# Kernel optimization log

Hardware: AMD Instinct MI355X
Metric: run time of the kernel (lower is better)

Reference implementation:

```python
import jax, jax.numpy as jnp
import numpy as np

TOKEN_SIZE = 4
NEIGHBOR_SIZE = 3


def setup_inputs() -> dict:
    key = jax.random.key(0)
    ks = jax.random.split(key, 8)
    B, C, H, W = 8, 256, 64, 64
    return {
        "blue_feat": jax.random.normal(ks[0], (B, C, H, W), jnp.float32),
        "white_feat": jax.random.normal(ks[1], (B, C, H, W), jnp.float32),
        "Wq": jax.random.normal(ks[2], (C, C), jnp.float32) * 0.05,
        "bq": jax.random.normal(ks[3], (C,), jnp.float32) * 0.05,
        "Wk": jax.random.normal(ks[4], (C, C), jnp.float32) * 0.05,
        "bk": jax.random.normal(ks[5], (C,), jnp.float32) * 0.05,
        "Wv": jax.random.normal(ks[6], (C, C), jnp.float32) * 0.05,
        "bv": jax.random.normal(ks[7], (C,), jnp.float32) * 0.05,
    }


def _tokens(x, nh, nw, ts):
    # [B,C,H,W] -> [B,nh,nw,C,ts*ts]
    B, C = x.shape[0], x.shape[1]
    return (x.reshape(B, C, nh, ts, nw, ts)
             .transpose(0, 2, 4, 1, 3, 5)
             .reshape(B, nh, nw, C, ts * ts))


def reference(blue_feat, white_feat, Wq, bq, Wk, bk, Wv, bv):
    ts, ns = TOKEN_SIZE, NEIGHBOR_SIZE
    pad = ns // 2
    B, C, H, W = blue_feat.shape
    scale = float((ts * ts) ** -0.5)

    # 1x1 conv projections (pointwise channel mix + bias)
    Q = jnp.einsum('bchw,oc->bohw', blue_feat, Wq) + bq[None, :, None, None]
    K = jnp.einsum('bchw,oc->bohw', white_feat, Wk) + bk[None, :, None, None]
    V = jnp.einsum('bchw,oc->bohw', white_feat, Wv) + bv[None, :, None, None]

    nh, nw = H // ts, W // ts  # H,W divisible by ts -> no padding branch
    Qt = _tokens(Q, nh, nw, ts)  # [B,nh,nw,C,D]
    Kt = _tokens(K, nh, nw, ts)
    Vt = _tokens(V, nh, nw, ts)

    # zero-padded token grid, gather 3x3 neighbor tokens (F.unfold equivalent)
    padw = ((0, 0), (pad, pad), (pad, pad), (0, 0), (0, 0))
    Kp = jnp.pad(Kt, padw)
    Vp = jnp.pad(Vt, padw)
    Knb = jnp.stack([Kp[:, di:di + nh, dj:dj + nw]
                     for di in range(ns) for dj in range(ns)], axis=3)  # [B,nh,nw,9,C,D]
    Vnb = jnp.stack([Vp[:, di:di + nh, dj:dj + nw]
                     for di in range(ns) for dj in range(ns)], axis=3)

    # per-channel attention over neighbor tokens
    attn = jax.nn.softmax(
        jnp.einsum('bhwcd,bhwncd->bhwcn', Qt, Knb) * scale, axis=-1)
    out = jnp.einsum('bhwcn,bhwncd->bhwcd', attn, Vnb)  # [B,nh,nw,C,D]

    enhanced = (out.reshape(B, nh, nw, C, ts, ts)
                   .transpose(0, 3, 1, 4, 2, 5)
                   .reshape(B, C, H, W))
    return blue_feat + enhanced  # out_proj is Identity since c1 == c2
```

## Files before the change

### kernel.cpp

```cpp
#include <hip/hip_runtime.h>
#include <hip/hip_bf16.h>
#include <stdint.h>

typedef float  f32x4  __attribute__((ext_vector_type(4)));
typedef float  f32x2  __attribute__((ext_vector_type(2)));
typedef __bf16 bf16x8 __attribute__((ext_vector_type(8)));

#define LROW 40

__global__ __launch_bounds__(1024) void prep_kernel(
    const float* __restrict__ blue, const float* __restrict__ white,
    const float* __restrict__ Wq, const float* __restrict__ Wk,
    const float* __restrict__ Wv,
    __bf16* __restrict__ Xtb, __bf16* __restrict__ Xtw,
    __bf16* __restrict__ Wbf)
{
  const int bid = blockIdx.x;
  const int tid = threadIdx.x;

  if (bid >= 256) {
    const int t = bid - 256;
    const float* src = (t == 0) ? Wq : (t == 1) ? Wk : Wv;
    __bf16* dst = Wbf + t * 65536;
#pragma unroll
    for (int it = 0; it < 8; ++it) {
      const int idx = it * 8192 + tid * 8;
      f32x4 v0 = *(const f32x4*)(src + idx);
      f32x4 v1 = *(const f32x4*)(src + idx + 4);
      bf16x8 r;
#pragma unroll
      for (int q = 0; q < 4; ++q) { r[q] = (__bf16)v0[q]; r[q + 4] = (__bf16)v1[q]; }
      *(bf16x8*)(dst + idx) = r;
    }
    return;
  }

  const int srcw = bid >> 7;
  const int rem  = bid & 127;
  const int b    = rem >> 4;
  const int ti   = rem & 15;
  const float* X = srcw ? white : blue;
  __bf16*     Xt = srcw ? Xtw : Xtb;

  const int s  = tid & 7;
  const int co = (tid >> 3) & 31;
  const int u  = tid >> 8;

  const float* Xb = X + (size_t)b * (256 * 4096);
  __bf16* Xtb2 = Xt + (size_t)b * 4096 * 256;

#pragma unroll
  for (int it = 0; it < 4; ++it) {
    const int p   = u * 32 + it * 8 + s;
    const int px  = 2 * p;
    const int r   = px >> 6;
    const int col = px & 63;
    const int hw  = (ti * 4 + r) * 64 + col;
    const int d   = r * 4 + (col & 3);
    const int n   = ti * 256 + (col >> 2) * 16 + d;

    bf16x8 e0, e1;
#pragma unroll
    for (int j = 0; j < 8; ++j) {
      const int c = co * 8 + j;
      f32x2 v = *(const f32x2*)(Xb + (size_t)c * 4096 + hw);
      e0[j] = (__bf16)v[0];
      e1[j] = (__bf16)v[1];
    }
    *(bf16x8*)(Xtb2 + (size_t)n * 256 + co * 8)       = e0;
    *(bf16x8*)(Xtb2 + (size_t)(n + 1) * 256 + co * 8) = e1;
  }
}


#define GLOAD16(GS, LD) \
  __builtin_amdgcn_global_load_lds( \
      (const __attribute__((address_space(1))) uint32_t*)(GS), \
      (__attribute__((address_space(3))) uint32_t*)(LD), 16, 0, 0)

__global__ __launch_bounds__(256) void gemm_lds_kernel(
    const __bf16* __restrict__ Xtb, const __bf16* __restrict__ Xtw,
    const __bf16* __restrict__ Wbf,
    const float* __restrict__ bq, const float* __restrict__ bk,
    const float* __restrict__ bv,
    __bf16* __restrict__ Qt, __bf16* __restrict__ Kt, __bf16* __restrict__ Vt)
{
  __shared__ __bf16 As[3][128 * 32];
  __shared__ __bf16 Bs[3][128 * 32];

  const int bid = blockIdx.x;
  const int lid = (bid & 7) * 192 + (bid >> 3);
  const int nb  = lid / 6;
  const int bt  = lid % 6;
  const int tensor = (bt < 4) ? 1 + (bt & 1) : 0;
  const int ob     = (bt < 4) ? (bt >> 1) : (bt & 1);

  const __bf16* Xt   = (tensor == 0) ? Xtb : Xtw;
  const float*  bias = (tensor == 0) ? bq : (tensor == 1) ? bk : bv;
  __bf16*       Out  = (tensor == 0) ? Qt : (tensor == 1) ? Kt : Vt;
  const __bf16* Wp   = Wbf + tensor * 65536 + ob * 32768;

  const int tid  = threadIdx.x;
  const int lane = tid & 63;
  const int w    = tid >> 6;
  const int wo   = w >> 1;
  const int wn   = w & 1;
  const int lrow = lane & 15;
  const int lks  = lane >> 4;

  const int o0 = ob * 128;
  const int n0 = nb * 128;

  const int l     = lane;
  const int rA    = w * 16 + (l >> 2);
  const int gslot = (l & 3) ^ ((l >> 3) & 3);
  const __bf16* gA = Wp + (size_t)rA * 256 + gslot * 8;
  const __bf16* gB = Xt + (size_t)(n0 + rA) * 256 + gslot * 8;
  const int ldsOffQ0 = (w * 16) * 32;
  const int ldsOffQ1 = (64 + w * 16) * 32;

#define STAGE(BUF, KK) do {                                        \
    GLOAD16(gA + (KK) * 32,             &As[BUF][ldsOffQ0]);       \
    GLOAD16(gA + 64 * 256 + (KK) * 32,  &As[BUF][ldsOffQ1]);       \
    GLOAD16(gB + (KK) * 32,             &Bs[BUF][ldsOffQ0]);       \
    GLOAD16(gB + 64 * 256 + (KK) * 32,  &Bs[BUF][ldsOffQ1]);       \
  } while (0)

  const int sx = ((lks ^ ((lrow >> 1) & 3)) * 8);

  f32x4 acc[4][4];
#pragma unroll
  for (int i = 0; i < 4; ++i)
#pragma unroll
    for (int j = 0; j < 4; ++j) acc[i][j] = (f32x4)0.0f;

#define COMPUTE(BUF) do {                                                       \
    bf16x8 af[4], bfr[4];                                                       \
    _Pragma("unroll")                                                           \
    for (int i = 0; i < 4; ++i)                                                 \
      af[i] = *(const bf16x8*)&As[BUF][(wo * 64 + i * 16 + lrow) * 32 + sx];    \
    _Pragma("unroll")                                                           \
    for (int j = 0; j < 4; ++j)                                                 \
      bfr[j] = *(const bf16x8*)&Bs[BUF][(wn * 64 + j * 16 + lrow) * 32 + sx];   \
    __builtin_amdgcn_s_setprio(1);                                              \
    _Pragma("unroll")                                                           \
    for (int i = 0; i < 4; ++i)                                                 \
      _Pragma("unroll")                                                         \
      for (int j = 0; j < 4; ++j)                                               \
        acc[i][j] = __builtin_amdgcn_mfma_f32_16x16x32_bf16(af[i], bfr[j],      \
                                                            acc[i][j], 0, 0, 0);\
    __builtin_amdgcn_s_setprio(0);                                              \
  } while (0)

  STAGE(0, 0);
  STAGE(1, 1);
  STAGE(2, 2);

#define PHASE(T) do {                                                           \
    if ((T) >= 6) {                                                             \
      if ((T) == 6) asm volatile("s_waitcnt vmcnt(4)" ::: "memory");            \
      else          asm volatile("s_waitcnt vmcnt(0)" ::: "memory");            \
    } else          asm volatile("s_waitcnt vmcnt(8)" ::: "memory");            \
    __builtin_amdgcn_sched_barrier(0);                                          \
    __builtin_amdgcn_s_barrier();                                               \
    __builtin_amdgcn_sched_barrier(0);                                          \
    COMPUTE((T) % 3);                                                           \
    asm volatile("s_waitcnt lgkmcnt(0)" ::: "memory");                          \
    __builtin_amdgcn_sched_barrier(0);                                          \
    __builtin_amdgcn_s_barrier();                                               \
    __builtin_amdgcn_sched_barrier(0);                                          \
    if ((T) < 5) STAGE((T) % 3, (T) + 3);                                       \
  } while (0)

  PHASE(0); PHASE(1); PHASE(2); PHASE(3);
  PHASE(4); PHASE(5); PHASE(6); PHASE(7);
#undef PHASE
#undef STAGE
#undef COMPUTE

#pragma unroll
  for (int i = 0; i < 4; ++i) {
    const int obase = o0 + wo * 64 + i * 16 + (lane >> 4) * 4;
#pragma unroll
    for (int j = 0; j < 4; ++j) {
      const int n  = n0 + wn * 64 + j * 16 + (lane & 15);
      const int bb = n >> 12;
      const int pp = n & 4095;
      const int tt = pp >> 4;
      const int tii = tt >> 4;
      const int tjj = tt & 15;
      const int dd  = pp & 15;
      const size_t base = ((size_t)(bb * 16 + tii) * 256) * 256 + tjj * 16 + dd;
#pragma unroll
      for (int r = 0; r < 4; ++r) {
        const int o = obase + r;
        const float v = acc[i][j][r] + bias[o];
        Out[base + (size_t)o * 256] = (__bf16)v;
      }
    }
  }
}

__global__ __launch_bounds__(256) void proj_gemm_kernel(
    const float* __restrict__ blue, const float* __restrict__ white,
    const float* __restrict__ Wq, const float* __restrict__ bq,
    const float* __restrict__ Wk, const float* __restrict__ bk,
    const float* __restrict__ Wv, const float* __restrict__ bv,
    __bf16* __restrict__ Qt, __bf16* __restrict__ Kt, __bf16* __restrict__ Vt)
{
  __shared__ __bf16 As[128 * LROW];
  __shared__ __bf16 Bs[128 * LROW];

  const int bidhw = blockIdx.x;
  const int lid   = (bidhw & 7) * 192 + (bidhw >> 3);
  const int nb    = lid / 6;
  const int bt    = lid % 6;
  const int tensor = (bt < 4) ? 1 + (bt & 1) : 0;
  const int ob     = (bt < 4) ? (bt >> 1) : (bt & 1);

  const float* X    = (tensor == 0) ? blue : white;
  const float* W    = (tensor == 0) ? Wq : (tensor == 1) ? Wk : Wv;
  const float* bias = (tensor == 0) ? bq : (tensor == 1) ? bk : bv;
  __bf16*      Out  = (tensor == 0) ? Qt : (tensor == 1) ? Kt : Vt;

  const int tid  = threadIdx.x;
  const int lane = tid & 63;
  const int wave = tid >> 6;
  const int wo   = wave >> 1;
  const int wn   = wave & 1;

  const int o0 = ob * 128;
  const int n0 = nb * 128;
  const int batch = n0 >> 12;
  const int p0    = n0 & 4095;
  const int tk0   = p0 >> 4;
  const int trow  = tk0 >> 4;
  const int tcol0 = tk0 & 15;
  const float* Xb = X + (size_t)batch * (256 * 4096);

  f32x4 acc[4][4];
#pragma unroll
  for (int i = 0; i < 4; ++i)
#pragma unroll
    for (int j = 0; j < 4; ++j) acc[i][j] = (f32x4)0.0f;

  const int arow  = tid >> 1;
  const int ahalf = tid & 1;
  const int n2   = tid & 63;
  const int ko   = tid >> 6;
  const int nloc = 2 * n2;
  const int tl   = nloc >> 4;
  const int d    = nloc & 15;
  const int hw   = (trow * 4 + (d >> 2)) * 64 + (tcol0 + tl) * 4 + (d & 3);

  const int lrow = lane & 15;
  const int lk   = (lane >> 4) * 8;

  for (int kk = 0; kk < 8; ++kk) {
    const int k0 = kk * 32;
    {
      const float* src = W + (size_t)(o0 + arow) * 256 + k0 + ahalf * 16;
      f32x4 t0 = *(const f32x4*)(src + 0);
      f32x4 t1 = *(const f32x4*)(src + 4);
      f32x4 t2 = *(const f32x4*)(src + 8);
      f32x4 t3 = *(const f32x4*)(src + 12);
      bf16x8 c0, c1;
#pragma unroll
      for (int qq = 0; qq < 4; ++qq) { c0[qq] = (__bf16)t0[qq]; c0[qq + 4] = (__bf16)t1[qq]; }
#pragma unroll
      for (int qq = 0; qq < 4; ++qq) { c1[qq] = (__bf16)t2[qq]; c1[qq + 4] = (__bf16)t3[qq]; }
      __bf16* dst = As + arow * LROW + ahalf * 16;
      *(bf16x8*)(dst + 0) = c0;
      *(bf16x8*)(dst + 8) = c1;
    }
    {
      const float* src = Xb + (size_t)(k0 + ko * 8) * 4096 + hw;
      f32x2 v0 = *(const f32x2*)(src + 0 * 4096);
      f32x2 v1 = *(const f32x2*)(src + 1 * 4096);
      f32x2 v2 = *(const f32x2*)(src + 2 * 4096);
      f32x2 v3 = *(const f32x2*)(src + 3 * 4096);
      f32x2 v4 = *(const f32x2*)(src + 4 * 4096);
      f32x2 v5 = *(const f32x2*)(src + 5 * 4096);
      f32x2 v6 = *(const f32x2*)(src + 6 * 4096);
      f32x2 v7 = *(const f32x2*)(src + 7 * 4096);
      bf16x8 r0, r1;
      r0[0] = (__bf16)v0[0]; r0[1] = (__bf16)v1[0]; r0[2] = (__bf16)v2[0]; r0[3] = (__bf16)v3[0];
      r0[4] = (__bf16)v4[0]; r0[5] = (__bf16)v5[0]; r0[6] = (__bf16)v6[0]; r0[7] = (__bf16)v7[0];
      r1[0] = (__bf16)v0[1]; r1[1] = (__bf16)v1[1]; r1[2] = (__bf16)v2[1]; r1[3] = (__bf16)v3[1];
      r1[4] = (__bf16)v4[1]; r1[5] = (__bf16)v5[1]; r1[6] = (__bf16)v6[1]; r1[7] = (__bf16)v7[1];
      *(bf16x8*)(Bs + (nloc + 0) * LROW + ko * 8) = r0;
      *(bf16x8*)(Bs + (nloc + 1) * LROW + ko * 8) = r1;
    }
    __syncthreads();

    bf16x8 a[4], b[4];
#pragma unroll
    for (int i = 0; i < 4; ++i)
      a[i] = *(const bf16x8*)(As + (wo * 64 + i * 16 + lrow) * LROW + lk);
#pragma unroll
    for (int j = 0; j < 4; ++j)
      b[j] = *(const bf16x8*)(Bs + (wn * 64 + j * 16 + lrow) * LROW + lk);
#pragma unroll
    for (int i = 0; i < 4; ++i)
#pragma unroll
      for (int j = 0; j < 4; ++j)
        acc[i][j] = __builtin_amdgcn_mfma_f32_16x16x32_bf16(a[i], b[j], acc[i][j], 0, 0, 0);
    __syncthreads();
  }

#pragma unroll
  for (int i = 0; i < 4; ++i) {
    const int obase = o0 + wo * 64 + i * 16 + (lane >> 4) * 4;
#pragma unroll
    for (int j = 0; j < 4; ++j) {
      const int n  = n0 + wn * 64 + j * 16 + (lane & 15);
      const int bb = n >> 12;
      const int p  = n & 4095;
      const int tt = p >> 4;
      const int tii = tt >> 4;
      const int tjj = tt & 15;
      const int dd  = p & 15;
      const size_t base = ((size_t)(bb * 16 + tii) * 256) * 256 + tjj * 16 + dd;
#pragma unroll
      for (int r = 0; r < 4; ++r) {
        const int o = obase + r;
        const float v = acc[i][j][r] + bias[o];
        Out[base + (size_t)o * 256] = (__bf16)v;
      }
    }
  }
}

__device__ __forceinline__ void unpack8(const uint4 v, float* f) {
  const uint32_t u0 = v.x, u1 = v.y, u2 = v.z, u3 = v.w;
  f[0] = __uint_as_float(u0 << 16); f[1] = __uint_as_float(u0 & 0xffff0000u);
  f[2] = __uint_as_float(u1 << 16); f[3] = __uint_as_float(u1 & 0xffff0000u);
  f[4] = __uint_as_float(u2 << 16); f[5] = __uint_as_float(u2 & 0xffff0000u);
  f[6] = __uint_as_float(u3 << 16); f[7] = __uint_as_float(u3 & 0xffff0000u);
}

__global__ __launch_bounds__(256) void attn_kernel(
    const __bf16* __restrict__ Qt, const __bf16* __restrict__ Kt,
    const __bf16* __restrict__ Vt, const float* __restrict__ blue,
    float* __restrict__ out)
{
  const int j   = blockIdx.x;
  const int bid = (j & 7) * 256 + (j >> 3);
  const int cg  = bid & 15;
  const int ti  = (bid >> 4) & 15;
  const int b   = bid >> 8;

  const int tid = threadIdx.x;
  const int tj  = tid & 15;
  const int cl  = tid >> 4;
  const int c   = cg * 16 + cl;

  float q[16];
  {
    const __bf16* p = Qt + ((((size_t)b * 16 + ti) * 256 + c) * 16 + tj) * 16;
    unpack8(*(const uint4*)p, q);
    unpack8(*(const uint4*)(p + 8), q + 8);
  }

  float s[9];
#pragma unroll
  for (int n = 0; n < 9; ++n) {
    const int yi = ti + n / 3 - 1;
    const int yj = tj + n % 3 - 1;
    float dot = 0.0f;
    if (yi >= 0 && yi < 16 && yj >= 0 && yj < 16) {
      const __bf16* p = Kt + ((((size_t)b * 16 + yi) * 256 + c) * 16 + yj) * 16;
      float kf[16];
      unpack8(*(const uint4*)p, kf);
      unpack8(*(const uint4*)(p + 8), kf + 8);
#pragma unroll
      for (int dd = 0; dd < 16; ++dd) dot = fmaf(q[dd], kf[dd], dot);
    }
    s[n] = dot * 0.25f;
  }

  float m = s[0];
#pragma unroll
  for (int n = 1; n < 9; ++n) m = fmaxf(m, s[n]);
  float w[9], denom = 0.0f;
#pragma unroll
  for (int n = 0; n < 9; ++n) { w[n] = __expf(s[n] - m); denom += w[n]; }
  const float inv = 1.0f / denom;

  float o16[16];
#pragma unroll
  for (int dd = 0; dd < 16; ++dd) o16[dd] = 0.0f;
#pragma unroll
  for (int n = 0; n < 9; ++n) {
    const int yi = ti + n / 3 - 1;
    const int yj = tj + n % 3 - 1;
    if (yi >= 0 && yi < 16 && yj >= 0 && yj < 16) {
      const __bf16* p = Vt + ((((size_t)b * 16 + yi) * 256 + c) * 16 + yj) * 16;
      float vf[16];
      unpack8(*(const uint4*)p, vf);
      unpack8(*(const uint4*)(p + 8), vf + 8);
#pragma unroll
      for (int dd = 0; dd < 16; ++dd) o16[dd] = fmaf(w[n], vf[dd], o16[dd]);
    }
  }

  const size_t pbase = ((size_t)b * 256 + c) * 4096 + (size_t)(ti * 4) * 64 + tj * 4;
#pragma unroll
  for (int r = 0; r < 4; ++r) {
    f32x4 bl = *(const f32x4*)(blue + pbase + r * 64);
    f32x4 ov;
#pragma unroll
    for (int j2 = 0; j2 < 4; ++j2) ov[j2] = bl[j2] + o16[r * 4 + j2] * inv;
    *(f32x4*)(out + pbase + r * 64) = ov;
  }
}

extern "C" void kernel_launch(void* const* d_in, const int* in_sizes, int n_in,
                              void* d_out, int out_size, void* d_ws, size_t ws_size,
                              hipStream_t stream) {
  const float* blue  = (const float*)d_in[0];
  const float* white = (const float*)d_in[1];
  const float* Wq = (const float*)d_in[2];
  const float* bq = (const float*)d_in[3];
  const float* Wk = (const float*)d_in[4];
  const float* bk = (const float*)d_in[5];
  const float* Wv = (const float*)d_in[6];
  const float* bv = (const float*)d_in[7];
  float* out = (float*)d_out;

  const size_t tsz = (size_t)8 * 256 * 256 * 16;
  const size_t xsz = (size_t)8 * 4096 * 256;
  __bf16* Qt = (__bf16*)d_ws;
  __bf16* Kt = Qt + tsz;
  __bf16* Vt = Kt + tsz;

  const size_t need_new = (3 * tsz + 2 * xsz + 3 * 65536) * sizeof(__bf16);
  if (ws_size >= need_new) {
    __bf16* Xtb = Vt + tsz;
    __bf16* Xtw = Xtb + xsz;
    __bf16* Wbf = Xtw + xsz;
    prep_kernel<<<259, 1024, 0, stream>>>(blue, white, Wq, Wk, Wv, Xtb, Xtw, Wbf);
    gemm_lds_kernel<<<1536, 256, 0, stream>>>(Xtb, Xtw, Wbf, bq, bk, bv, Qt, Kt, Vt);
  } else {
    proj_gemm_kernel<<<1536, 256, 0, stream>>>(blue, white, Wq, bq, Wk, bk, Wv, bv, Qt, Kt, Vt);
  }
  attn_kernel<<<2048, 256, 0, stream>>>(Qt, Kt, Vt, blue, out);
}
```

Before: 70.76 us.

## Fuse activation transpose and bf16 cast into GEMM via fp32 LDS staging

Removes the separate prep pass that transposed and converted the blue/white activations to bf16 in a workspace. The GEMM now loads fp32 activations directly from the NCHW layout into LDS with global_load_lds and converts to bf16 while building MFMA fragments. A small kernel still converts only the weights. This avoids an extra round trip of the activations through global memory, at the cost of twice the LDS footprint for the B tile, more LDS reads per fragment with scalar conversions, and more outstanding loads per stage.

```diff
diff --git a/kernel.cpp b/kernel.cpp
--- a/kernel.cpp
+++ b/kernel.cpp
@@ -8,68 +8,20 @@
 
 #define LROW 40
 
-__global__ __launch_bounds__(1024) void prep_kernel(
-    const float* __restrict__ blue, const float* __restrict__ white,
+__global__ __launch_bounds__(256) void wprep_kernel(
     const float* __restrict__ Wq, const float* __restrict__ Wk,
-    const float* __restrict__ Wv,
-    __bf16* __restrict__ Xtb, __bf16* __restrict__ Xtw,
-    __bf16* __restrict__ Wbf)
+    const float* __restrict__ Wv, __bf16* __restrict__ Wbf)
 {
-  const int bid = blockIdx.x;
-  const int tid = threadIdx.x;
-
-  if (bid >= 256) {
-    const int t = bid - 256;
-    const float* src = (t == 0) ? Wq : (t == 1) ? Wk : Wv;
-    __bf16* dst = Wbf + t * 65536;
-#pragma unroll
-    for (int it = 0; it < 8; ++it) {
-      const int idx = it * 8192 + tid * 8;
-      f32x4 v0 = *(const f32x4*)(src + idx);
-      f32x4 v1 = *(const f32x4*)(src + idx + 4);
-      bf16x8 r;
-#pragma unroll
-      for (int q = 0; q < 4; ++q) { r[q] = (__bf16)v0[q]; r[q + 4] = (__bf16)v1[q]; }
-      *(bf16x8*)(dst + idx) = r;
-    }
-    return;
-  }
-
-  const int srcw = bid >> 7;
-  const int rem  = bid & 127;
-  const int b    = rem >> 4;
-  const int ti   = rem & 15;
-  const float* X = srcw ? white : blue;
-  __bf16*     Xt = srcw ? Xtw : Xtb;
-
-  const int s  = tid & 7;
-  const int co = (tid >> 3) & 31;
-  const int u  = tid >> 8;
-
-  const float* Xb = X + (size_t)b * (256 * 4096);
-  __bf16* Xtb2 = Xt + (size_t)b * 4096 * 256;
-
-#pragma unroll
-  for (int it = 0; it < 4; ++it) {
-    const int p   = u * 32 + it * 8 + s;
-    const int px  = 2 * p;
-    const int r   = px >> 6;
-    const int col = px & 63;
-    const int hw  = (ti * 4 + r) * 64 + col;
-    const int d   = r * 4 + (col & 3);
-    const int n   = ti * 256 + (col >> 2) * 16 + d;
-
-    bf16x8 e0, e1;
-#pragma unroll
-    for (int j = 0; j < 8; ++j) {
-      const int c = co * 8 + j;
-      f32x2 v = *(const f32x2*)(Xb + (size_t)c * 4096 + hw);
-      e0[j] = (__bf16)v[0];
-      e1[j] = (__bf16)v[1];
-    }
-    *(bf16x8*)(Xtb2 + (size_t)n * 256 + co * 8)       = e0;
-    *(bf16x8*)(Xtb2 + (size_t)(n + 1) * 256 + co * 8) = e1;
-  }
+  const int wb = blockIdx.x;
+  const int t  = wb >> 5;
+  const float* src = (t == 0) ? Wq : (t == 1) ? Wk : Wv;
+  const int off = (wb & 31) * 2048 + threadIdx.x * 8;
+  f32x4 v0 = *(const f32x4*)(src + off);
+  f32x4 v1 = *(const f32x4*)(src + off + 4);
+  bf16x8 r;
+#pragma unroll
+  for (int q = 0; q < 4; ++q) { r[q] = (__bf16)v0[q]; r[q + 4] = (__bf16)v1[q]; }
+  *(bf16x8*)(Wbf + t * 65536 + off) = r;
 }
 
 
@@ -78,15 +30,15 @@
       (const __attribute__((address_space(1))) uint32_t*)(GS), \
       (__attribute__((address_space(3))) uint32_t*)(LD), 16, 0, 0)
 
-__global__ __launch_bounds__(256) void gemm_lds_kernel(
-    const __bf16* __restrict__ Xtb, const __bf16* __restrict__ Xtw,
+__global__ __launch_bounds__(256) void gemm_f32lds_kernel(
+    const float* __restrict__ blue, const float* __restrict__ white,
     const __bf16* __restrict__ Wbf,
     const float* __restrict__ bq, const float* __restrict__ bk,
     const float* __restrict__ bv,
     __bf16* __restrict__ Qt, __bf16* __restrict__ Kt, __bf16* __restrict__ Vt)
 {
+  __shared__ float  Bsf[3][32 * 128];
   __shared__ __bf16 As[3][128 * 32];
-  __shared__ __bf16 Bs[3][128 * 32];
 
   const int bid = blockIdx.x;
   const int lid = (bid & 7) * 192 + (bid >> 3);
@@ -95,7 +47,7 @@
   const int tensor = (bt < 4) ? 1 + (bt & 1) : 0;
   const int ob     = (bt < 4) ? (bt >> 1) : (bt & 1);
 
-  const __bf16* Xt   = (tensor == 0) ? Xtb : Xtw;
+  const float*  X    = (tensor == 0) ? blue : white;
   const float*  bias = (tensor == 0) ? bq : (tensor == 1) ? bk : bv;
   __bf16*       Out  = (tensor == 0) ? Qt : (tensor == 1) ? Kt : Vt;
   const __bf16* Wp   = Wbf + tensor * 65536 + ob * 32768;
@@ -108,25 +60,45 @@
   const int lrow = lane & 15;
   const int lks  = lane >> 4;
 
-  const int o0 = ob * 128;
-  const int n0 = nb * 128;
-
-  const int l     = lane;
-  const int rA    = w * 16 + (l >> 2);
-  const int gslot = (l & 3) ^ ((l >> 3) & 3);
+  const int o0    = ob * 128;
+  const int n0    = nb * 128;
+  const int batch = n0 >> 12;
+  const int p0    = n0 & 4095;
+  const int tk0   = p0 >> 4;
+  const int trow  = tk0 >> 4;
+  const int tcol0 = tk0 & 15;
+  const float* Xb = X + (size_t)batch * (256 * 4096);
+
+  const float* gB[4];
+#pragma unroll
+  for (int m = 0; m < 4; ++m) {
+    const int c      = m * 4 + w;
+    const int krow   = 2 * c + (lane >> 5);
+    const int g      = c >> 2;
+    const int px_src = ((lane & 31) * 4 + 16 * g) & 127;
+    const int tl     = px_src >> 4;
+    const int d      = px_src & 15;
+    const int hw     = (trow * 4 + (d >> 2)) * 64 + (tcol0 + tl) * 4 + (d & 3);
+    gB[m] = Xb + (size_t)krow * 4096 + hw;
+  }
+
+  const int rA    = w * 16 + (lane >> 2);
+  const int gslot = (lane & 3) ^ ((lane >> 3) & 3);
   const __bf16* gA = Wp + (size_t)rA * 256 + gslot * 8;
-  const __bf16* gB = Xt + (size_t)(n0 + rA) * 256 + gslot * 8;
   const int ldsOffQ0 = (w * 16) * 32;
   const int ldsOffQ1 = (64 + w * 16) * 32;
 
-#define STAGE(BUF, KK) do {                                        \
-    GLOAD16(gA + (KK) * 32,             &As[BUF][ldsOffQ0]);       \
-    GLOAD16(gA + 64 * 256 + (KK) * 32,  &As[BUF][ldsOffQ1]);       \
-    GLOAD16(gB + (KK) * 32,             &Bs[BUF][ldsOffQ0]);       \
-    GLOAD16(gB + 64 * 256 + (KK) * 32,  &Bs[BUF][ldsOffQ1]);       \
+#define STAGE(BUF, KK) do {                                          \
+    GLOAD16(gA + (KK) * 32,            &As[BUF][ldsOffQ0]);          \
+    GLOAD16(gA + 64 * 256 + (KK) * 32, &As[BUF][ldsOffQ1]);          \
+    GLOAD16(gB[0] + (size_t)(KK) * 32 * 4096, &Bsf[BUF][(0 * 4 + w) * 256]); \
+    GLOAD16(gB[1] + (size_t)(KK) * 32 * 4096, &Bsf[BUF][(1 * 4 + w) * 256]); \
+    GLOAD16(gB[2] + (size_t)(KK) * 32 * 4096, &Bsf[BUF][(2 * 4 + w) * 256]); \
+    GLOAD16(gB[3] + (size_t)(KK) * 32 * 4096, &Bsf[BUF][(3 * 4 + w) * 256]); \
   } while (0)
 
-  const int sx = ((lks ^ ((lrow >> 1) & 3)) * 8);
+  const int sxA = (lks ^ ((lrow >> 1) & 3)) * 8;
+  const int pxb = wn * 64 + lrow;
 
   f32x4 acc[4][4];
 #pragma unroll
@@ -138,10 +110,16 @@
     bf16x8 af[4], bfr[4];                                                       \
     _Pragma("unroll")                                                           \
     for (int i = 0; i < 4; ++i)                                                 \
-      af[i] = *(const bf16x8*)&As[BUF][(wo * 64 + i * 16 + lrow) * 32 + sx];    \
+      af[i] = *(const bf16x8*)&As[BUF][(wo * 64 + i * 16 + lrow) * 32 + sxA];   \
     _Pragma("unroll")                                                           \
-    for (int j = 0; j < 4; ++j)                                                 \
-      bfr[j] = *(const bf16x8*)&Bs[BUF][(wn * 64 + j * 16 + lrow) * 32 + sx];   \
+    for (int j = 0; j < 4; ++j) {                                               \
+      const int s = (pxb + j * 16 - 16 * lks + 128) & 127;                      \
+      const float* bp = &Bsf[BUF][lks * 8 * 128 + s];                           \
+      bf16x8 v;                                                                 \
+      _Pragma("unroll")                                                         \
+      for (int kk = 0; kk < 8; ++kk) v[kk] = (__bf16)bp[kk * 128];              \
+      bfr[j] = v;                                                               \
+    }                                                                           \
     __builtin_amdgcn_s_setprio(1);                                              \
     _Pragma("unroll")                                                           \
     for (int i = 0; i < 4; ++i)                                                 \
@@ -157,10 +135,9 @@
   STAGE(2, 2);
 
 #define PHASE(T) do {                                                           \
-    if ((T) >= 6) {                                                             \
-      if ((T) == 6) asm volatile("s_waitcnt vmcnt(4)" ::: "memory");            \
-      else          asm volatile("s_waitcnt vmcnt(0)" ::: "memory");            \
-    } else          asm volatile("s_waitcnt vmcnt(8)" ::: "memory");            \
+    if ((T) == 7)      asm volatile("s_waitcnt vmcnt(0)"  ::: "memory");        \
+    else if ((T) == 6) asm volatile("s_waitcnt vmcnt(6)"  ::: "memory");        \
+    else               asm volatile("s_waitcnt vmcnt(12)" ::: "memory");        \
     __builtin_amdgcn_sched_barrier(0);                                          \
     __builtin_amdgcn_s_barrier();                                               \
     __builtin_amdgcn_sched_barrier(0);                                          \
@@ -429,18 +406,15 @@
   float* out = (float*)d_out;
 
   const size_t tsz = (size_t)8 * 256 * 256 * 16;
-  const size_t xsz = (size_t)8 * 4096 * 256;
   __bf16* Qt = (__bf16*)d_ws;
   __bf16* Kt = Qt + tsz;
   __bf16* Vt = Kt + tsz;
 
-  const size_t need_new = (3 * tsz + 2 * xsz + 3 * 65536) * sizeof(__bf16);
-  if (ws_size >= need_new) {
-    __bf16* Xtb = Vt + tsz;
-    __bf16* Xtw = Xtb + xsz;
-    __bf16* Wbf = Xtw + xsz;
-    prep_kernel<<<259, 1024, 0, stream>>>(blue, white, Wq, Wk, Wv, Xtb, Xtw, Wbf);
-    gemm_lds_kernel<<<1536, 256, 0, stream>>>(Xtb, Xtw, Wbf, bq, bk, bv, Qt, Kt, Vt);
+  const size_t need = (3 * tsz + 3 * 65536) * sizeof(__bf16);
+  if (ws_size >= need) {
+    __bf16* Wbf = Vt + tsz;
+    wprep_kernel<<<96, 256, 0, stream>>>(Wq, Wk, Wv, Wbf);
+    gemm_f32lds_kernel<<<1536, 256, 0, stream>>>(blue, white, Wbf, bq, bk, bv, Qt, Kt, Vt);
   } else {
     proj_gemm_kernel<<<1536, 256, 0, stream>>>(blue, white, Wq, bq, Wk, bk, Wv, bv, Qt, Kt, Vt);
   }
```

Measured after the change: 72.69 us. 1.03x slower.

## Switch projection GEMM to BK=64 double-buffered LDS pipeline with 8-slot XOR swizzle

Applied to the files above, without the earlier changes.

The projection GEMM now stages 64-wide K tiles into two LDS buffers instead of 32-wide tiles into three. That halves the number of K iterations and barrier pairs from 8 to 4. The load addressing and LDS swizzle are rebuilt for 64-element rows using an XOR over 8 slots, and each compute step consumes two K=32 halves. LDS per block grows from 48KB to 64KB, which may lower occupancy and shortens how far loads are prefetched ahead.

```diff
diff --git a/kernel.cpp b/kernel.cpp
--- a/kernel.cpp
+++ b/kernel.cpp
@@ -78,15 +78,15 @@
       (const __attribute__((address_space(1))) uint32_t*)(GS), \
       (__attribute__((address_space(3))) uint32_t*)(LD), 16, 0, 0)
 
-__global__ __launch_bounds__(256) void gemm_lds_kernel(
+__global__ __launch_bounds__(256) void gemm_bk64_kernel(
     const __bf16* __restrict__ Xtb, const __bf16* __restrict__ Xtw,
     const __bf16* __restrict__ Wbf,
     const float* __restrict__ bq, const float* __restrict__ bk,
     const float* __restrict__ bv,
     __bf16* __restrict__ Qt, __bf16* __restrict__ Kt, __bf16* __restrict__ Vt)
 {
-  __shared__ __bf16 As[3][128 * 32];
-  __shared__ __bf16 Bs[3][128 * 32];
+  __shared__ __bf16 As[2][128 * 64];
+  __shared__ __bf16 Bs[2][128 * 64];
 
   const int bid = blockIdx.x;
   const int lid = (bid & 7) * 192 + (bid >> 3);
@@ -111,23 +111,31 @@
   const int o0 = ob * 128;
   const int n0 = nb * 128;
 
-  const int l     = lane;
-  const int rA    = w * 16 + (l >> 2);
-  const int gslot = (l & 3) ^ ((l >> 3) & 3);
-  const __bf16* gA = Wp + (size_t)rA * 256 + gslot * 8;
-  const __bf16* gB = Xt + (size_t)(n0 + rA) * 256 + gslot * 8;
-  const int ldsOffQ0 = (w * 16) * 32;
-  const int ldsOffQ1 = (64 + w * 16) * 32;
+  const __bf16* gAsrc[4];
+  const __bf16* gBsrc[4];
+  int ldsOff[4];
+#pragma unroll
+  for (int m = 0; m < 4; ++m) {
+    const int i    = w * 4 + m;
+    const int row  = i * 8 + (lane >> 3);
+    const int slot = lane & 7;
+    const int ps   = slot ^ (row & 7);
+    gAsrc[m]  = Wp + (size_t)row * 256 + ps * 8;
+    gBsrc[m]  = Xt + (size_t)(n0 + row) * 256 + ps * 8;
+    ldsOff[m] = i * 512;
+  }
 
 #define STAGE(BUF, KK) do {                                        \
-    GLOAD16(gA + (KK) * 32,             &As[BUF][ldsOffQ0]);       \
-    GLOAD16(gA + 64 * 256 + (KK) * 32,  &As[BUF][ldsOffQ1]);       \
-    GLOAD16(gB + (KK) * 32,             &Bs[BUF][ldsOffQ0]);       \
-    GLOAD16(gB + 64 * 256 + (KK) * 32,  &Bs[BUF][ldsOffQ1]);       \
+    GLOAD16(gAsrc[0] + (KK) * 64, &As[BUF][ldsOff[0]]);            \
+    GLOAD16(gAsrc[1] + (KK) * 64, &As[BUF][ldsOff[1]]);            \
+    GLOAD16(gAsrc[2] + (KK) * 64, &As[BUF][ldsOff[2]]);            \
+    GLOAD16(gAsrc[3] + (KK) * 64, &As[BUF][ldsOff[3]]);            \
+    GLOAD16(gBsrc[0] + (KK) * 64, &Bs[BUF][ldsOff[0]]);            \
+    GLOAD16(gBsrc[1] + (KK) * 64, &Bs[BUF][ldsOff[1]]);            \
+    GLOAD16(gBsrc[2] + (KK) * 64, &Bs[BUF][ldsOff[2]]);            \
+    GLOAD16(gBsrc[3] + (KK) * 64, &Bs[BUF][ldsOff[3]]);            \
   } while (0)
 
-  const int sx = ((lks ^ ((lrow >> 1) & 3)) * 8);
-
   f32x4 acc[4][4];
 #pragma unroll
   for (int i = 0; i < 4; ++i)
@@ -135,46 +143,53 @@
     for (int j = 0; j < 4; ++j) acc[i][j] = (f32x4)0.0f;
 
 #define COMPUTE(BUF) do {                                                       \
-    bf16x8 af[4], bfr[4];                                                       \
     _Pragma("unroll")                                                           \
-    for (int i = 0; i < 4; ++i)                                                 \
-      af[i] = *(const bf16x8*)&As[BUF][(wo * 64 + i * 16 + lrow) * 32 + sx];    \
-    _Pragma("unroll")                                                           \
-    for (int j = 0; j < 4; ++j)                                                 \
-      bfr[j] = *(const bf16x8*)&Bs[BUF][(wn * 64 + j * 16 + lrow) * 32 + sx];   \
-    __builtin_amdgcn_s_setprio(1);                                              \
-    _Pragma("unroll")                                                           \
-    for (int i = 0; i < 4; ++i)                                                 \
+    for (int h = 0; h < 2; ++h) {                                               \
+      bf16x8 af[4], bfr[4];                                                     \
       _Pragma("unroll")                                                         \
-      for (int j = 0; j < 4; ++j)                                               \
-        acc[i][j] = __builtin_amdgcn_mfma_f32_16x16x32_bf16(af[i], bfr[j],      \
-                                                            acc[i][j], 0, 0, 0);\
-    __builtin_amdgcn_s_setprio(0);                                              \
+      for (int i = 0; i < 4; ++i) {                                             \
+        const int row = wo * 64 + i * 16 + lrow;                                \
+        af[i] = *(const bf16x8*)&As[BUF][row * 64 +                             \
+                   (((h * 4 + lks) ^ (row & 7)) * 8)];                          \
+      }                                                                         \
+      _Pragma("unroll")                                                         \
+      for (int j = 0; j < 4; ++j) {                                             \
+        const int row = wn * 64 + j * 16 + lrow;                                \
+        bfr[j] = *(const bf16x8*)&Bs[BUF][row * 64 +                            \
+                   (((h * 4 + lks) ^ (row & 7)) * 8)];                          \
+      }                                                                         \
+      __builtin_amdgcn_s_setprio(1);                                            \
+      _Pragma("unroll")                                                         \
+      for (int i = 0; i < 4; ++i)                                               \
+        _Pragma("unroll")                                                       \
+        for (int j = 0; j < 4; ++j)                                             \
+          acc[i][j] = __builtin_amdgcn_mfma_f32_16x16x32_bf16(af[i], bfr[j],    \
+                                                              acc[i][j], 0,0,0);\
+      __builtin_amdgcn_s_setprio(0);                                            \
+    }                                                                           \
   } while (0)
 
-  STAGE(0, 0);
-  STAGE(1, 1);
-  STAGE(2, 2);
-
-#define PHASE(T) do {                                                           \
-    if ((T) >= 6) {                                                             \
-      if ((T) == 6) asm volatile("s_waitcnt vmcnt(4)" ::: "memory");            \
-      else          asm volatile("s_waitcnt vmcnt(0)" ::: "memory");            \
-    } else          asm volatile("s_waitcnt vmcnt(8)" ::: "memory");            \
+#define WAITBAR(N) do {                                                         \
+    asm volatile("s_waitcnt vmcnt(" #N ")" ::: "memory");                       \
     __builtin_amdgcn_sched_barrier(0);                                          \
     __builtin_amdgcn_s_barrier();                                               \
     __builtin_amdgcn_sched_barrier(0);                                          \
-    COMPUTE((T) % 3);                                                           \
+  } while (0)
+
+#define ENDBAR() do {                                                           \
     asm volatile("s_waitcnt lgkmcnt(0)" ::: "memory");                          \
     __builtin_amdgcn_sched_barrier(0);                                          \
     __builtin_amdgcn_s_barrier();                                               \
     __builtin_amdgcn_sched_barrier(0);                                          \
-    if ((T) < 5) STAGE((T) % 3, (T) + 3);                                       \
   } while (0)
 
-  PHASE(0); PHASE(1); PHASE(2); PHASE(3);
-  PHASE(4); PHASE(5); PHASE(6); PHASE(7);
-#undef PHASE
+  STAGE(0, 0);
+  STAGE(1, 1);  WAITBAR(8);  COMPUTE(0);  ENDBAR();
+  STAGE(0, 2);  WAITBAR(8);  COMPUTE(1);  ENDBAR();
+  STAGE(1, 3);  WAITBAR(8);  COMPUTE(0);  ENDBAR();
+                WAITBAR(0);  COMPUTE(1);
+#undef WAITBAR
+#undef ENDBAR
 #undef STAGE
 #undef COMPUTE
 
@@ -434,13 +449,13 @@
   __bf16* Kt = Qt + tsz;
   __bf16* Vt = Kt + tsz;
 
-  const size_t need_new = (3 * tsz + 2 * xsz + 3 * 65536) * sizeof(__bf16);
-  if (ws_size >= need_new) {
+  const size_t need = (3 * tsz + 2 * xsz + 3 * 65536) * sizeof(__bf16);
+  if (ws_size >= need) {
     __bf16* Xtb = Vt + tsz;
     __bf16* Xtw = Xtb + xsz;
     __bf16* Wbf = Xtw + xsz;
     prep_kernel<<<259, 1024, 0, stream>>>(blue, white, Wq, Wk, Wv, Xtb, Xtw, Wbf);
-    gemm_lds_kernel<<<1536, 256, 0, stream>>>(Xtb, Xtw, Wbf, bq, bk, bv, Qt, Kt, Vt);
+    gemm_bk64_kernel<<<1536, 256, 0, stream>>>(Xtb, Xtw, Wbf, bq, bk, bv, Qt, Kt, Vt);
   } else {
     proj_gemm_kernel<<<1536, 256, 0, stream>>>(blue, white, Wq, bq, Wk, bk, Wv, bv, Qt, Kt, Vt);
   }
```

New measurement: 71.08 us. About the same (+0.5%).
